# Optimization experiments

Measured on AMD Instinct MI355X. Metric: run time of the kernel, lower is better.

## Reference

```python
import jax, jax.numpy as jnp
import numpy as np


def setup_inputs() -> dict:
    key = jax.random.key(0)
    ks = jax.random.split(key, 4)
    B, C, H, W = 8, 64, 256, 256
    return {
        "x": jax.random.normal(ks[0], (B, C, H, W), jnp.float32),
        "fc_w": jax.random.normal(ks[1], (C, C), jnp.float32) / np.sqrt(C).astype(np.float32),
        "fc_b": jnp.zeros((C,), jnp.float32),
        "conv1_w": jax.random.normal(ks[2], (2,), jnp.float32),  # [mean_ch, max_ch] of 1x1 conv
        "conv1_b": jnp.zeros((1,), jnp.float32),
        "conv2_w": jax.random.normal(ks[3], (2,), jnp.float32),
        "conv2_b": jnp.zeros((1,), jnp.float32),
        "size": 4,
    }


def reference(x, fc_w, fc_b, conv1_w, conv1_b, conv2_w, conv2_b, size):
    B, C, H, W = x.shape
    s = size
    h, w = H // s, W // s
    # unfold (non-overlapping) -> [B, L, C, s*s], L = h*w, patch pixels row-major
    p = x.reshape(B, C, h, s, w, s).transpose(0, 2, 4, 1, 3, 5).reshape(B, h * w, C, s * s)
    # channel attention: max over patch pixels -> fc -> sigmoid
    m = jax.nn.sigmoid(jnp.max(p, axis=3) @ fc_w.T + fc_b)  # [B, L, C]
    p = p * m[..., None]
    # spatial-in-patch attention: (mean, max) over channel axis -> 1x1 conv(2->1) -> sigmoid
    g1 = jax.nn.sigmoid(
        conv1_w[0] * jnp.mean(p, axis=2, keepdims=True)
        + conv1_w[1] * jnp.max(p, axis=2, keepdims=True)
        + conv1_b[0]
    )  # [B, L, 1, s*s]
    p = p * g1
    # fold back to [B, C, H, W]
    y = p.reshape(B, h, w, C, s, s).transpose(0, 3, 1, 4, 2, 5).reshape(B, C, H, W)
    # per-patch gating: (mean, max) over all C*s*s values of each patch
    yb = y.reshape(B, C, h, s, w, s)
    mx = jnp.max(yb, axis=(1, 3, 5))   # [B, h, w]
    mn = jnp.mean(yb, axis=(1, 3, 5))  # [B, h, w]
    g2 = jax.nn.sigmoid(conv2_w[0] * mn + conv2_w[1] * mx + conv2_b[0])
    g2 = jnp.repeat(jnp.repeat(g2, s, axis=1), s, axis=2)  # [B, H, W]
    return y * g2[:, None, :, :]
```

## Files before the change

### kernel.cpp

```cpp
#include <hip/hip_runtime.h>
#include <math.h>

constexpr int Bc = 8, Cc = 64, Hc = 256, Wc = 256, Sc = 4;
constexpr int PHn = Hc / Sc;
constexpr int PWn = Wc / Sc;
constexpr int NPATCH = Bc * PHn * PWn;
constexpr int WPB = 4;

__device__ __forceinline__ float sigmoidf_(float v) {
    return 1.0f / (1.0f + __expf(-v));
}

__global__ __launch_bounds__(256, 4)
void ciam_kernel(const float* __restrict__ x,
                 const float* __restrict__ fc_w,
                 const float* __restrict__ fc_b,
                 const float* __restrict__ c1w,
                 const float* __restrict__ c1b,
                 const float* __restrict__ c2w,
                 const float* __restrict__ c2b,
                 float* __restrict__ out)
{
    __shared__ float fcw_lds[64 * 65];
    __shared__ float maxbuf[WPB][64];
    __shared__ float pixbuf[WPB][16 * 65];
    __shared__ float g1buf[WPB][16];

    const int tid  = threadIdx.x;
    const int wave = tid >> 6;
    const int lane = tid & 63;

    #pragma unroll
    for (int i = 0; i < 16; ++i) {
        int idx = tid + i * 256;
        fcw_lds[(idx >> 6) * 65 + (idx & 63)] = fc_w[idx];
    }

    const float w10 = c1w[0], w11 = c1w[1], b1 = c1b[0];
    const float w20 = c2w[0], w21 = c2w[1], b2 = c2b[0];

    const int patch = blockIdx.x * WPB + wave;
    const int b  = patch >> 12;
    const int l  = patch & 4095;
    const int ph = l >> 6;
    const int pw = l & 63;
    const int c  = lane;

    const size_t base = ((size_t)(b * Cc + c) * Hc + ph * Sc) * Wc + pw * Sc;

    float4 v[4];
    #pragma unroll
    for (int i = 0; i < 4; ++i)
        v[i] = *reinterpret_cast<const float4*>(x + base + (size_t)i * Wc);

    float mv = -3.4e38f;
    #pragma unroll
    for (int i = 0; i < 4; ++i)
        mv = fmaxf(mv, fmaxf(fmaxf(v[i].x, v[i].y), fmaxf(v[i].z, v[i].w)));
    maxbuf[wave][lane] = mv;
    __syncthreads();

    float acc = fc_b[c];
    #pragma unroll 16
    for (int k = 0; k < 64; ++k)
        acc = fmaf(fcw_lds[c * 65 + k], maxbuf[wave][k], acc);
    const float m = sigmoidf_(acc);

    #pragma unroll
    for (int i = 0; i < 4; ++i) {
        v[i].x *= m; v[i].y *= m; v[i].z *= m; v[i].w *= m;
    }

    #pragma unroll
    for (int i = 0; i < 4; ++i) {
        pixbuf[wave][(i * 4 + 0) * 65 + c] = v[i].x;
        pixbuf[wave][(i * 4 + 1) * 65 + c] = v[i].y;
        pixbuf[wave][(i * 4 + 2) * 65 + c] = v[i].z;
        pixbuf[wave][(i * 4 + 3) * 65 + c] = v[i].w;
    }
    __syncthreads();

    {
        const int a = lane >> 2, q = lane & 3;
        const float* pb = &pixbuf[wave][a * 65 + q * 16];
        float s = 0.f, mx = -3.4e38f;
        #pragma unroll
        for (int t = 0; t < 16; ++t) {
            float u = pb[t];
            s += u;
            mx = fmaxf(mx, u);
        }
        s  += __shfl_xor(s, 1);
        s  += __shfl_xor(s, 2);
        mx  = fmaxf(mx, __shfl_xor(mx, 1));
        mx  = fmaxf(mx, __shfl_xor(mx, 2));
        float g1 = sigmoidf_(w10 * (s * (1.f / 64.f)) + w11 * mx + b1);
        if (q == 0) g1buf[wave][a] = g1;
    }
    __syncthreads();

    #pragma unroll
    for (int i = 0; i < 4; ++i) {
        v[i].x *= g1buf[wave][i * 4 + 0];
        v[i].y *= g1buf[wave][i * 4 + 1];
        v[i].z *= g1buf[wave][i * 4 + 2];
        v[i].w *= g1buf[wave][i * 4 + 3];
    }

    float ls = 0.f, lmx = -3.4e38f;
    #pragma unroll
    for (int i = 0; i < 4; ++i) {
        ls += v[i].x + v[i].y + v[i].z + v[i].w;
        lmx = fmaxf(lmx, fmaxf(fmaxf(v[i].x, v[i].y), fmaxf(v[i].z, v[i].w)));
    }
    #pragma unroll
    for (int off = 32; off >= 1; off >>= 1) {
        ls  += __shfl_xor(ls, off);
        lmx  = fmaxf(lmx, __shfl_xor(lmx, off));
    }
    const float g2 = sigmoidf_(w20 * (ls * (1.f / 1024.f)) + w21 * lmx + b2);

    #pragma unroll
    for (int i = 0; i < 4; ++i) {
        float4 o = v[i];
        o.x *= g2; o.y *= g2; o.z *= g2; o.w *= g2;
        *reinterpret_cast<float4*>(out + base + (size_t)i * Wc) = o;
    }
}

extern "C" void kernel_launch(void* const* d_in, const int* in_sizes, int n_in,
                              void* d_out, int out_size, void* d_ws, size_t ws_size,
                              hipStream_t stream) {
    const float* x    = (const float*)d_in[0];
    const float* fc_w = (const float*)d_in[1];
    const float* fc_b = (const float*)d_in[2];
    const float* c1w  = (const float*)d_in[3];
    const float* c1b  = (const float*)d_in[4];
    const float* c2w  = (const float*)d_in[5];
    const float* c2b  = (const float*)d_in[6];

    float* out = (float*)d_out;
    ciam_kernel<<<NPATCH / WPB, 256, 0, stream>>>(x, fc_w, fc_b, c1w, c1b, c2w, c2b, out);
}
```

Baseline: 299.9 us.

## Stage 8-patch column tiles through LDS for coalesced global loads and stores

Each block now processes eight horizontally adjacent patches, loading a 64-channel by 4-row by 32-column tile with contiguous float4 reads into padded shared memory, then transposing into per-channel registers. Each wave handles two patches, sharing the FC weight reads across both. Results are written back through shared memory so global stores are also contiguous. This targets the scattered 16-byte per-lane accesses of the old layout, at the cost of much larger LDS use, which lowers occupancy, and extra barriers.

```diff
diff --git a/kernel.cpp b/kernel.cpp
--- a/kernel.cpp
+++ b/kernel.cpp
@@ -2,16 +2,16 @@
 #include <math.h>
 
 constexpr int Bc = 8, Cc = 64, Hc = 256, Wc = 256, Sc = 4;
-constexpr int PHn = Hc / Sc;
-constexpr int PWn = Wc / Sc;
-constexpr int NPATCH = Bc * PHn * PWn;
-constexpr int WPB = 4;
+constexpr int NPATCH = Bc * (Hc / Sc) * (Wc / Sc);
+constexpr int TP = 8;
+constexpr int CPITCH = 133;
+constexpr int RPITCH = 33;
 
 __device__ __forceinline__ float sigmoidf_(float v) {
     return 1.0f / (1.0f + __expf(-v));
 }
 
-__global__ __launch_bounds__(256, 4)
+__global__ __launch_bounds__(256, 2)
 void ciam_kernel(const float* __restrict__ x,
                  const float* __restrict__ fc_w,
                  const float* __restrict__ fc_b,
@@ -21,110 +21,149 @@
                  const float* __restrict__ c2b,
                  float* __restrict__ out)
 {
+    __shared__ float T[64 * CPITCH];
     __shared__ float fcw_lds[64 * 65];
-    __shared__ float maxbuf[WPB][64];
-    __shared__ float pixbuf[WPB][16 * 65];
-    __shared__ float g1buf[WPB][16];
+    __shared__ float maxbuf[TP][64];
+    __shared__ float pixbuf[4][16 * 65];
+    __shared__ float g1buf[4][2][16];
 
     const int tid  = threadIdx.x;
-    const int wave = tid >> 6;
-    const int lane = tid & 63;
+    const int gid  = blockIdx.x;
+    const int b    = gid >> 9;
+    const int rem  = gid & 511;
+    const int ph   = rem >> 3;
+    const int pwg  = rem & 7;
+    const int col0 = pwg * 32;
 
     #pragma unroll
-    for (int i = 0; i < 16; ++i) {
-        int idx = tid + i * 256;
-        fcw_lds[(idx >> 6) * 65 + (idx & 63)] = fc_w[idx];
+    for (int i = 0; i < 4; ++i) {
+        int u   = i * 256 + tid;
+        int row = u >> 4;
+        int jf  = (u & 15) << 2;
+        const float4 wv = *reinterpret_cast<const float4*>(fc_w + row * 64 + jf);
+        float* fd = &fcw_lds[row * 65 + jf];
+        fd[0] = wv.x; fd[1] = wv.y; fd[2] = wv.z; fd[3] = wv.w;
+    }
+
+    #pragma unroll
+    for (int i = 0; i < 8; ++i) {
+        int u   = i * 256 + tid;
+        int seg = u >> 3;
+        int c_  = seg >> 2;
+        int r_  = seg & 3;
+        int j4  = (u & 7) << 2;
+        const float4 val = *reinterpret_cast<const float4*>(
+            x + (((size_t)(b * Cc + c_) * Hc + (ph * Sc + r_)) * Wc + col0 + j4));
+        float* td = &T[c_ * CPITCH + r_ * RPITCH + j4];
+        td[0] = val.x; td[1] = val.y; td[2] = val.z; td[3] = val.w;
     }
 
     const float w10 = c1w[0], w11 = c1w[1], b1 = c1b[0];
     const float w20 = c2w[0], w21 = c2w[1], b2 = c2b[0];
 
-    const int patch = blockIdx.x * WPB + wave;
-    const int b  = patch >> 12;
-    const int l  = patch & 4095;
-    const int ph = l >> 6;
-    const int pw = l & 63;
-    const int c  = lane;
-
-    const size_t base = ((size_t)(b * Cc + c) * Hc + ph * Sc) * Wc + pw * Sc;
-
-    float4 v[4];
-    #pragma unroll
-    for (int i = 0; i < 4; ++i)
-        v[i] = *reinterpret_cast<const float4*>(x + base + (size_t)i * Wc);
-
-    float mv = -3.4e38f;
-    #pragma unroll
-    for (int i = 0; i < 4; ++i)
-        mv = fmaxf(mv, fmaxf(fmaxf(v[i].x, v[i].y), fmaxf(v[i].z, v[i].w)));
-    maxbuf[wave][lane] = mv;
     __syncthreads();
 
-    float acc = fc_b[c];
+    const int wave = tid >> 6;
+    const int lane = tid & 63;
+    const int c    = lane;
+    const int p0   = wave * 2;
+
+    float v[2][16];
+    #pragma unroll
+    for (int pi = 0; pi < 2; ++pi) {
+        const float* tp = &T[c * CPITCH + (p0 + pi) * 4];
+        #pragma unroll
+        for (int r = 0; r < 4; ++r)
+            #pragma unroll
+            for (int j = 0; j < 4; ++j)
+                v[pi][r * 4 + j] = tp[r * RPITCH + j];
+    }
+
+    float mx0 = -3.4e38f, mx1 = -3.4e38f;
+    #pragma unroll
+    for (int t = 0; t < 16; ++t) {
+        mx0 = fmaxf(mx0, v[0][t]);
+        mx1 = fmaxf(mx1, v[1][t]);
+    }
+    maxbuf[p0][c]     = mx0;
+    maxbuf[p0 + 1][c] = mx1;
+    __syncthreads();
+
+    float a0 = fc_b[c], a1 = a0;
     #pragma unroll 16
-    for (int k = 0; k < 64; ++k)
-        acc = fmaf(fcw_lds[c * 65 + k], maxbuf[wave][k], acc);
-    const float m = sigmoidf_(acc);
+    for (int k = 0; k < 64; ++k) {
+        float wv = fcw_lds[c * 65 + k];
+        a0 = fmaf(wv, maxbuf[p0][k], a0);
+        a1 = fmaf(wv, maxbuf[p0 + 1][k], a1);
+    }
+    const float m0 = sigmoidf_(a0), m1 = sigmoidf_(a1);
+    #pragma unroll
+    for (int t = 0; t < 16; ++t) { v[0][t] *= m0; v[1][t] *= m1; }
 
     #pragma unroll
-    for (int i = 0; i < 4; ++i) {
-        v[i].x *= m; v[i].y *= m; v[i].z *= m; v[i].w *= m;
+    for (int pi = 0; pi < 2; ++pi) {
+        #pragma unroll
+        for (int t = 0; t < 16; ++t)
+            pixbuf[wave][t * 65 + c] = v[pi][t];
+        __syncthreads();
+        {
+            const int a = lane >> 2, q = lane & 3;
+            const float* pb = &pixbuf[wave][a * 65 + q * 16];
+            float s = 0.f, mxp = -3.4e38f;
+            #pragma unroll
+            for (int t = 0; t < 16; ++t) {
+                float u = pb[t];
+                s += u;
+                mxp = fmaxf(mxp, u);
+            }
+            s   += __shfl_xor(s, 1);
+            s   += __shfl_xor(s, 2);
+            mxp  = fmaxf(mxp, __shfl_xor(mxp, 1));
+            mxp  = fmaxf(mxp, __shfl_xor(mxp, 2));
+            float g1 = sigmoidf_(w10 * (s * (1.f / 64.f)) + w11 * mxp + b1);
+            if (q == 0) g1buf[wave][pi][a] = g1;
+        }
+        __syncthreads();
+        #pragma unroll
+        for (int t = 0; t < 16; ++t)
+            v[pi][t] *= g1buf[wave][pi][t];
     }
 
     #pragma unroll
-    for (int i = 0; i < 4; ++i) {
-        pixbuf[wave][(i * 4 + 0) * 65 + c] = v[i].x;
-        pixbuf[wave][(i * 4 + 1) * 65 + c] = v[i].y;
-        pixbuf[wave][(i * 4 + 2) * 65 + c] = v[i].z;
-        pixbuf[wave][(i * 4 + 3) * 65 + c] = v[i].w;
-    }
-    __syncthreads();
-
-    {
-        const int a = lane >> 2, q = lane & 3;
-        const float* pb = &pixbuf[wave][a * 65 + q * 16];
-        float s = 0.f, mx = -3.4e38f;
+    for (int pi = 0; pi < 2; ++pi) {
+        float ls = 0.f, lmx = -3.4e38f;
         #pragma unroll
         for (int t = 0; t < 16; ++t) {
-            float u = pb[t];
-            s += u;
-            mx = fmaxf(mx, u);
+            ls += v[pi][t];
+            lmx = fmaxf(lmx, v[pi][t]);
         }
-        s  += __shfl_xor(s, 1);
-        s  += __shfl_xor(s, 2);
-        mx  = fmaxf(mx, __shfl_xor(mx, 1));
-        mx  = fmaxf(mx, __shfl_xor(mx, 2));
-        float g1 = sigmoidf_(w10 * (s * (1.f / 64.f)) + w11 * mx + b1);
-        if (q == 0) g1buf[wave][a] = g1;
+        #pragma unroll
+        for (int off = 32; off >= 1; off >>= 1) {
+            ls  += __shfl_xor(ls, off);
+            lmx  = fmaxf(lmx, __shfl_xor(lmx, off));
+        }
+        const float g2 = sigmoidf_(w20 * (ls * (1.f / 1024.f)) + w21 * lmx + b2);
+        float* tp = &T[c * CPITCH + (p0 + pi) * 4];
+        #pragma unroll
+        for (int r = 0; r < 4; ++r)
+            #pragma unroll
+            for (int j = 0; j < 4; ++j)
+                tp[r * RPITCH + j] = v[pi][r * 4 + j] * g2;
     }
     __syncthreads();
 
     #pragma unroll
-    for (int i = 0; i < 4; ++i) {
-        v[i].x *= g1buf[wave][i * 4 + 0];
-        v[i].y *= g1buf[wave][i * 4 + 1];
-        v[i].z *= g1buf[wave][i * 4 + 2];
-        v[i].w *= g1buf[wave][i * 4 + 3];
-    }
-
-    float ls = 0.f, lmx = -3.4e38f;
-    #pragma unroll
-    for (int i = 0; i < 4; ++i) {
-        ls += v[i].x + v[i].y + v[i].z + v[i].w;
-        lmx = fmaxf(lmx, fmaxf(fmaxf(v[i].x, v[i].y), fmaxf(v[i].z, v[i].w)));
-    }
-    #pragma unroll
-    for (int off = 32; off >= 1; off >>= 1) {
-        ls  += __shfl_xor(ls, off);
-        lmx  = fmaxf(lmx, __shfl_xor(lmx, off));
-    }
-    const float g2 = sigmoidf_(w20 * (ls * (1.f / 1024.f)) + w21 * lmx + b2);
-
-    #pragma unroll
-    for (int i = 0; i < 4; ++i) {
-        float4 o = v[i];
-        o.x *= g2; o.y *= g2; o.z *= g2; o.w *= g2;
-        *reinterpret_cast<float4*>(out + base + (size_t)i * Wc) = o;
+    for (int i = 0; i < 8; ++i) {
+        int u   = i * 256 + tid;
+        int seg = u >> 3;
+        int c_  = seg >> 2;
+        int r_  = seg & 3;
+        int j4  = (u & 7) << 2;
+        const float* ts = &T[c_ * CPITCH + r_ * RPITCH + j4];
+        float4 o;
+        o.x = ts[0]; o.y = ts[1]; o.z = ts[2]; o.w = ts[3];
+        *reinterpret_cast<float4*>(
+            out + (((size_t)(b * Cc + c_) * Hc + (ph * Sc + r_)) * Wc + col0 + j4)) = o;
     }
 }
 
@@ -140,5 +179,5 @@
     const float* c2b  = (const float*)d_in[6];
 
     float* out = (float*)d_out;
-    ciam_kernel<<<NPATCH / WPB, 256, 0, stream>>>(x, fc_w, fc_b, c1w, c1b, c2w, c2b, out);
+    ciam_kernel<<<NPATCH / TP, 256, 0, stream>>>(x, fc_w, fc_b, c1w, c1b, c2w, c2b, out);
 }
```

After: 258.2 us. 1.16x faster.
